# Kernel optimization log

Hardware: AMD Instinct MI355X
Metric: run time of the kernel (lower is better)

Reference implementation:

```python
import jax, jax.numpy as jnp
import numpy as np

B, D, H = 8192, 512, 512


def _linear_init(key, out_dim, in_dim, bias=True):
    # torch nn.Linear default: U(-1/sqrt(in_dim), 1/sqrt(in_dim)) for W and b
    k1, k2 = jax.random.split(key)
    bound = 1.0 / np.sqrt(in_dim)
    W = jax.random.uniform(k1, (out_dim, in_dim), jnp.float32, -bound, bound)
    if not bias:
        return W
    b = jax.random.uniform(k2, (out_dim,), jnp.float32, -bound, bound)
    return W, b


def setup_inputs() -> dict:
    key = jax.random.key(0)
    ks = jax.random.split(key, 16)
    x = jax.random.normal(ks[0], (B, D), jnp.float32)
    delta_t = jax.random.uniform(ks[1], (B, 1), jnp.float32)
    hidden = jax.random.normal(ks[2], (B, H), jnp.float32)
    cell_s = jax.random.normal(ks[3], (B, H), jnp.float32)
    Wii, bii = _linear_init(ks[4], H, D)
    Whi, bhi = _linear_init(ks[5], H, H)
    Wig, big = _linear_init(ks[6], H, D)
    Whg, bhg = _linear_init(ks[7], H, H)
    Wio, bio = _linear_init(ks[8], H, D)
    Who, bho = _linear_init(ks[9], H, H)
    Wto, bto = _linear_init(ks[10], H, 1)
    Wco, bco = _linear_init(ks[11], H, H)
    Wit1, bit1 = _linear_init(ks[12], H, D)
    Wtt1 = _linear_init(ks[13], H, 1, bias=False)
    Wit2, bit2 = _linear_init(ks[14], H, D)
    Wtt2 = _linear_init(ks[15], H, 1, bias=False)
    return dict(x=x, delta_t=delta_t, hidden=hidden, cell_s=cell_s,
                Wii=Wii, bii=bii, Whi=Whi, bhi=bhi, Wig=Wig, big=big,
                Whg=Whg, bhg=bhg, Wio=Wio, bio=bio, Who=Who, bho=bho,
                Wto=Wto, bto=bto, Wco=Wco, bco=bco, Wit1=Wit1, bit1=bit1,
                Wtt1=Wtt1, Wit2=Wit2, bit2=bit2, Wtt2=Wtt2)


def _lin(a, W, b=None):
    y = a @ W.T
    return y if b is None else y + b


def reference(x, delta_t, hidden, cell_s,
              Wii, bii, Whi, bhi, Wig, big, Whg, bhg,
              Wio, bio, Who, bho, Wto, bto, Wco, bco,
              Wit1, bit1, Wtt1, Wit2, bit2, Wtt2):
    sig, tanh = jax.nn.sigmoid, jnp.tanh
    tm1 = sig(_lin(x, Wit1, bit1) + sig(_lin(delta_t, Wtt1)))
    tm2 = sig(_lin(x, Wit2, bit2) + sig(_lin(delta_t, Wtt2)))
    im = sig(_lin(x, Wii, bii) + _lin(hidden, Whi, bhi))
    cur_in = tanh(_lin(x, Wig, big) + _lin(hidden, Whg, bhg))
    it1 = im * tm1
    cm_t = (1.0 - it1) * cell_s + it1 * cur_in
    cm = (1.0 - im) * cell_s + im * tm2 * cur_in
    om = sig(_lin(x, Wio, bio) + _lin(delta_t, Wto, bto)
             + _lin(hidden, Who, bho) + _lin(cm_t, Wco, bco))
    hm = om * tanh(cm_t)
    return (hm, cm)
```

## Files before the change

kernel.cpp:

```cpp
#include <hip/hip_runtime.h>
#include <hip/hip_bf16.h>
#include <stdint.h>

#define B_SZ 8192
#define D_SZ 512
#define H_SZ 512
#define KC 1024
#define NPRE 2560

typedef __attribute__((ext_vector_type(8))) __bf16 bf16x8;
typedef __attribute__((ext_vector_type(4))) float f32x4;

__device__ __forceinline__ unsigned short f2bf(float f) {
  unsigned u = __builtin_bit_cast(unsigned, f);
  u += 0x7FFFu + ((u >> 16) & 1u);
  return (unsigned short)(u >> 16);
}
__device__ __forceinline__ float bf2f(unsigned short h) {
  unsigned u = ((unsigned)h) << 16;
  return __builtin_bit_cast(float, u);
}
__device__ __forceinline__ float sigf(float x) {
  return __builtin_amdgcn_rcpf(1.0f + __expf(-x));
}
__device__ __forceinline__ float tanh_fast(float x) {
  float e = __expf(-2.0f * x);
  return (1.0f - e) * __builtin_amdgcn_rcpf(1.0f + e);
}

__device__ __forceinline__ void async_ld16(const unsigned short* g, unsigned short* l) {
  __builtin_amdgcn_global_load_lds(
      (const __attribute__((address_space(1))) unsigned int*)g,
      (__attribute__((address_space(3))) unsigned int*)l, 16, 0, 0);
}

struct WSrcs { const float* wx[5]; const float* wh[3]; const float* wco; };

__global__ void pack_all(const float* __restrict__ x, const float* __restrict__ h, WSrcs ws,
                         unsigned short* __restrict__ Ab, unsigned short* __restrict__ Wall,
                         unsigned short* __restrict__ Wcob) {
  int i = (blockIdx.x * 256 + threadIdx.x) * 4;
  const int XH = B_SZ * KC;
  const float* s;
  unsigned short* d;
  if (i < XH) {
    int b = i >> 10, c = i & 1023;
    s = (c < 512) ? (x + (size_t)b * 512 + c) : (h + (size_t)b * 512 + (c - 512));
    d = Ab + i;
  } else if (i < XH + NPRE * KC) {
    int j = i - XH;
    int row = j >> 10, c = j & 1023;
    int gate = row >> 9, r = row & 511;
    d = Wall + j;
    if (c < 512) {
      s = ws.wx[gate] + (size_t)r * 512 + c;
    } else if (gate >= 2) {
      s = ws.wh[gate - 2] + (size_t)r * 512 + (c - 512);
    } else {
      return;
    }
  } else {
    int j = i - XH - NPRE * KC;
    s = ws.wco + j;
    d = Wcob + j;
  }
  float4 v = *(const float4*)s;
  ushort4 o; o.x = f2bf(v.x); o.y = f2bf(v.y); o.z = f2bf(v.z); o.w = f2bf(v.w);
  *(ushort4*)d = o;
}

__global__ __launch_bounds__(640, 2) void igo_gate(
    const unsigned short* __restrict__ A, const unsigned short* __restrict__ Wall,
    const float* __restrict__ delta_t, const float* __restrict__ cell_s,
    const float* __restrict__ bii, const float* __restrict__ bhi,
    const float* __restrict__ big, const float* __restrict__ bhg,
    const float* __restrict__ bio, const float* __restrict__ bho,
    const float* __restrict__ Wto, const float* __restrict__ bto,
    const float* __restrict__ bco,
    const float* __restrict__ bit1, const float* __restrict__ Wtt1,
    const float* __restrict__ bit2, const float* __restrict__ Wtt2,
    float* __restrict__ out_cm, unsigned short* __restrict__ cmt_b,
    unsigned short* __restrict__ ao_b) {
  __shared__ __align__(16) unsigned short sBuf[28672];
  const int tid  = threadIdx.x;
  const int wave = tid >> 6, lane = tid & 63;
  const int ln15 = lane & 15, kq = lane >> 4;
  const int mh   = wave / 5, slot = wave % 5;
  const long bm  = (long)blockIdx.y * 128;
  const int  bn64 = blockIdx.x * 64;

  f32x4 acc[4][4];
#pragma unroll
  for (int i = 0; i < 4; ++i)
#pragma unroll
    for (int j = 0; j < 4; ++j) acc[i][j] = (f32x4){0.f, 0.f, 0.f, 0.f};

  const int swb = ln15 & 7;
  bf16x8* chunks = (bf16x8*)sBuf;

  for (int kt = 0; kt < 16; ++kt) {
    const int k0 = kt << 6;
    __syncthreads();
    const int cnt = (kt < 8) ? 3584 : 2560;
    for (int idx = tid; idx < cnt; idx += 640) {
      int t_lin = idx >> 9;
      int f     = idx & 511;
      int tile  = (kt < 8) ? t_lin : (t_lin < 2 ? t_lin : t_lin + 2);
      int row = f >> 3;
      int col = ((f & 7) ^ (row & 7)) << 3;
      const unsigned short* src;
      if (tile < 2) src = A    + (size_t)(bm + tile * 64 + row) * KC + k0 + col;
      else          src = Wall + (size_t)((tile - 2) * 512 + bn64 + row) * KC + k0 + col;
      async_ld16(src, sBuf + (size_t)(tile * 512 + f) * 8);
    }
    __syncthreads();
    if (kt < 8 || slot >= 2) {
#pragma unroll
      for (int ko = 0; ko < 2; ++ko) {
        const int q = (ko * 4 + kq) ^ swb;
        bf16x8 af[4], wf[4];
#pragma unroll
        for (int t = 0; t < 4; ++t)
          af[t] = chunks[mh * 512 + (t * 16 + ln15) * 8 + q];
#pragma unroll
        for (int t = 0; t < 4; ++t)
          wf[t] = chunks[(2 + slot) * 512 + (t * 16 + ln15) * 8 + q];
#pragma unroll
        for (int i = 0; i < 4; ++i)
#pragma unroll
          for (int j = 0; j < 4; ++j)
            acc[i][j] = __builtin_amdgcn_mfma_f32_16x16x32_bf16(af[i], wf[j], acc[i][j], 0, 0, 0);
      }
    }
  }

  for (int mh_e = 0; mh_e < 2; ++mh_e) {
    __syncthreads();
    if (mh == mh_e) {
#pragma unroll
      for (int i = 0; i < 4; ++i)
#pragma unroll
        for (int j = 0; j < 4; ++j)
#pragma unroll
          for (int r = 0; r < 4; ++r) {
            int row = i * 16 + kq * 4 + r;
            int col = j * 16 + ln15;
            sBuf[(size_t)slot * 4096 + row * 64 + col] = f2bf(acc[i][j][r]);
          }
    }
    __syncthreads();
    for (int v = tid; v < 1024; v += 640) {
      int row = v >> 4;
      int c4  = (v & 15) << 2;
      long b  = bm + mh_e * 64 + row;
      int  h  = bn64 + c4;
      int  lo = row * 64 + c4;
      ushort4 ut1 = *(const ushort4*)(sBuf + 0 * 4096 + lo);
      ushort4 ut2 = *(const ushort4*)(sBuf + 1 * 4096 + lo);
      ushort4 uai = *(const ushort4*)(sBuf + 2 * 4096 + lo);
      ushort4 uag = *(const ushort4*)(sBuf + 3 * 4096 + lo);
      ushort4 uao = *(const ushort4*)(sBuf + 4 * 4096 + lo);
      float4 cs   = *(const float4*)(cell_s + (size_t)b * 512 + h);
      float4 vbii = *(const float4*)(bii + h), vbhi = *(const float4*)(bhi + h);
      float4 vbig = *(const float4*)(big + h), vbhg = *(const float4*)(bhg + h);
      float4 vbio = *(const float4*)(bio + h), vbho = *(const float4*)(bho + h);
      float4 vWto = *(const float4*)(Wto + h), vbto = *(const float4*)(bto + h);
      float4 vbco = *(const float4*)(bco + h);
      float4 vbt1 = *(const float4*)(bit1 + h), vwt1 = *(const float4*)(Wtt1 + h);
      float4 vbt2 = *(const float4*)(bit2 + h), vwt2 = *(const float4*)(Wtt2 + h);
      float dtb   = delta_t[b];

      float4 ocm; ushort4 ocmt, oao;
#pragma unroll
      for (int l = 0; l < 4; ++l) {
        float t1 = sigf(bf2f(((const unsigned short*)&ut1)[l]) + ((const float*)&vbt1)[l]
                        + sigf(dtb * ((const float*)&vwt1)[l]));
        float t2 = sigf(bf2f(((const unsigned short*)&ut2)[l]) + ((const float*)&vbt2)[l]
                        + sigf(dtb * ((const float*)&vwt2)[l]));
        float ai = bf2f(((const unsigned short*)&uai)[l]) + ((const float*)&vbii)[l] + ((const float*)&vbhi)[l];
        float ag = bf2f(((const unsigned short*)&uag)[l]) + ((const float*)&vbig)[l] + ((const float*)&vbhg)[l];
        float ao = bf2f(((const unsigned short*)&uao)[l]) + ((const float*)&vbio)[l] + ((const float*)&vbho)[l]
                 + dtb * ((const float*)&vWto)[l] + ((const float*)&vbto)[l] + ((const float*)&vbco)[l];
        float im = sigf(ai);
        float g  = tanh_fast(ag);
        float csl = ((const float*)&cs)[l];
        float it1 = im * t1;
        float cmt = (1.f - it1) * csl + it1 * g;
        float cm  = (1.f - im) * csl + im * t2 * g;
        ((float*)&ocm)[l] = cm;
        ((unsigned short*)&ocmt)[l] = f2bf(cmt);
        ((unsigned short*)&oao)[l]  = f2bf(ao);
      }
      *(float4*)(out_cm + (size_t)b * 512 + h) = ocm;
      *(ushort4*)(cmt_b + (size_t)b * 512 + h) = ocmt;
      *(ushort4*)(ao_b  + (size_t)b * 512 + h) = oao;
    }
  }
}

__global__ __launch_bounds__(256, 2) void gemm_out(
    const unsigned short* __restrict__ A , const unsigned short* __restrict__ W ,
    const unsigned short* __restrict__ AO, float* __restrict__ out_hm) {
  __shared__ bf16x8 sA[128 * 8];
  __shared__ bf16x8 sW[128 * 8];
  const int tid  = threadIdx.x;
  const int wave = tid >> 6, lane = tid & 63;
  const int ln15 = lane & 15, kq = lane >> 4;
  const int wr = wave >> 1, wc = wave & 1;
  const long bm = (long)blockIdx.y * 128;
  const long bn = (long)blockIdx.x * 128;
  const int swb = ln15 & 7;

  f32x4 acc[4][4];
#pragma unroll
  for (int i = 0; i < 4; ++i)
#pragma unroll
    for (int j = 0; j < 4; ++j) acc[i][j] = (f32x4){0.f, 0.f, 0.f, 0.f};

  for (int kt = 0; kt < 8; ++kt) {
    const int k0 = kt << 6;
    __syncthreads();
#pragma unroll
    for (int it = 0; it < 4; ++it) {
      int f   = it * 256 + tid;
      int row = f >> 3;
      int col = ((f & 7) ^ (row & 7)) << 3;
      int ldsc = it * 256 + wave * 64;
      async_ld16(A + (size_t)(bm + row) * H_SZ + k0 + col, (unsigned short*)sA + (size_t)ldsc * 8);
      async_ld16(W + (size_t)(bn + row) * H_SZ + k0 + col, (unsigned short*)sW + (size_t)ldsc * 8);
    }
    __syncthreads();
#pragma unroll
    for (int ko = 0; ko < 2; ++ko) {
      const int q = (ko * 4 + kq) ^ swb;
      bf16x8 af[4], wf[4];
#pragma unroll
      for (int t = 0; t < 4; ++t)
        af[t] = sA[(wr * 64 + t * 16 + ln15) * 8 + q];
#pragma unroll
      for (int t = 0; t < 4; ++t)
        wf[t] = sW[(wc * 64 + t * 16 + ln15) * 8 + q];
#pragma unroll
      for (int i = 0; i < 4; ++i)
#pragma unroll
        for (int j = 0; j < 4; ++j)
          acc[i][j] = __builtin_amdgcn_mfma_f32_16x16x32_bf16(af[i], wf[j], acc[i][j], 0, 0, 0);
    }
  }
#pragma unroll
  for (int i = 0; i < 4; ++i) {
    const long r0 = bm + wr * 64 + i * 16 + kq * 4;
#pragma unroll
    for (int j = 0; j < 4; ++j) {
      const long c = bn + wc * 64 + j * 16 + ln15;
#pragma unroll
      for (int r = 0; r < 4; ++r) {
        long row = r0 + r;
        size_t idx = (size_t)row * H_SZ + c;
        float ao  = bf2f(AO[idx]);
        float om  = sigf(ao + acc[i][j][r]);
        float cmt = bf2f(A[idx]);
        out_hm[idx] = om * tanh_fast(cmt);
      }
    }
  }
}

extern "C" void kernel_launch(void* const* d_in, const int* in_sizes, int n_in,
                              void* d_out, int out_size, void* d_ws, size_t ws_size,
                              hipStream_t stream) {
  const float* x    = (const float*)d_in[0];
  const float* dt   = (const float*)d_in[1];
  const float* hid  = (const float*)d_in[2];
  const float* cell = (const float*)d_in[3];
  const float* Wii  = (const float*)d_in[4];
  const float* bii  = (const float*)d_in[5];
  const float* Whi  = (const float*)d_in[6];
  const float* bhi  = (const float*)d_in[7];
  const float* Wig  = (const float*)d_in[8];
  const float* big  = (const float*)d_in[9];
  const float* Whg  = (const float*)d_in[10];
  const float* bhg  = (const float*)d_in[11];
  const float* Wio  = (const float*)d_in[12];
  const float* bio  = (const float*)d_in[13];
  const float* Who  = (const float*)d_in[14];
  const float* bho  = (const float*)d_in[15];
  const float* Wto  = (const float*)d_in[16];
  const float* bto  = (const float*)d_in[17];
  const float* Wco  = (const float*)d_in[18];
  const float* bco  = (const float*)d_in[19];
  const float* Wit1 = (const float*)d_in[20];
  const float* bit1 = (const float*)d_in[21];
  const float* Wtt1 = (const float*)d_in[22];
  const float* Wit2 = (const float*)d_in[23];
  const float* bit2 = (const float*)d_in[24];
  const float* Wtt2 = (const float*)d_in[25];

  char* wp = (char*)d_ws;
  unsigned short* Ab   = (unsigned short*)wp; wp += (size_t)B_SZ * KC * 2;
  unsigned short* Wall = (unsigned short*)wp; wp += (size_t)NPRE * KC * 2;
  unsigned short* Wcob = (unsigned short*)wp; wp += (size_t)H_SZ * H_SZ * 2;
  unsigned short* Cmtb = (unsigned short*)wp; wp += (size_t)B_SZ * H_SZ * 2;
  unsigned short* AOb  = (unsigned short*)wp; wp += (size_t)B_SZ * H_SZ * 2;

  float* out = (float*)d_out;

  WSrcs wsrc;
  wsrc.wx[0] = Wit1; wsrc.wx[1] = Wit2; wsrc.wx[2] = Wii; wsrc.wx[3] = Wig; wsrc.wx[4] = Wio;
  wsrc.wh[0] = Whi;  wsrc.wh[1] = Whg;  wsrc.wh[2] = Who; wsrc.wco = Wco;
  const int pack_elems = B_SZ * KC + NPRE * KC + H_SZ * H_SZ;
  pack_all<<<pack_elems / 4 / 256, 256, 0, stream>>>(x, hid, wsrc, Ab, Wall, Wcob);

  igo_gate<<<dim3(8, 64), 640, 0, stream>>>(
      Ab, Wall, dt, cell, bii, bhi, big, bhg, bio, bho, Wto, bto, bco,
      bit1, Wtt1, bit2, Wtt2,
      out + (size_t)B_SZ * H_SZ, Cmtb, AOb);

  gemm_out<<<dim3(4, 64), 256, 0, stream>>>(Cmtb, Wcob, AOb, out);
}
```

Baseline: 251.6 us.

## Retile gate GEMM to 64-row blocks with 4 waves and XCD-aware block mapping

The gate kernel goes from 640-thread blocks covering 128 rows and 5 gate tiles to 256-thread blocks covering 64 rows. Three waves each compute one full-K gate (i, g, o), and a fourth wave computes the two half-K time gates with two accumulator sets, which aims to balance MFMA work across waves and raise occupancy. Both GEMM kernels now use a 1D grid whose block index is remapped by XCD, so neighbouring row tiles share an L2 and reuse weights. In exchange, the A tile is reloaded per 64 rows rather than shared across 128 rows, and wave 3 holds twice the accumulator registers.

```diff
diff --git a/kernel.cpp b/kernel.cpp
--- a/kernel.cpp
+++ b/kernel.cpp
@@ -69,7 +69,7 @@
   *(ushort4*)d = o;
 }
 
-__global__ __launch_bounds__(640, 2) void igo_gate(
+__global__ __launch_bounds__(256, 3) void fused_gate(
     const unsigned short* __restrict__ A, const unsigned short* __restrict__ Wall,
     const float* __restrict__ delta_t, const float* __restrict__ cell_s,
     const float* __restrict__ bii, const float* __restrict__ bhi,
@@ -81,19 +81,24 @@
     const float* __restrict__ bit2, const float* __restrict__ Wtt2,
     float* __restrict__ out_cm, unsigned short* __restrict__ cmt_b,
     unsigned short* __restrict__ ao_b) {
-  __shared__ __align__(16) unsigned short sBuf[28672];
+  __shared__ __align__(16) unsigned short sBuf[24576];
   const int tid  = threadIdx.x;
   const int wave = tid >> 6, lane = tid & 63;
   const int ln15 = lane & 15, kq = lane >> 4;
-  const int mh   = wave / 5, slot = wave % 5;
-  const long bm  = (long)blockIdx.y * 128;
-  const int  bn64 = blockIdx.x * 64;
-
-  f32x4 acc[4][4];
+  const int bid  = blockIdx.x;
+  const int xcd  = bid & 7, idx0 = bid >> 3;
+  const long bm  = (long)(xcd * 16 + (idx0 >> 3)) * 64;
+  const int  bn64 = (idx0 & 7) * 64;
+
+  f32x4 acc_a[4][4];
+  f32x4 acc_b[4][4];
 #pragma unroll
   for (int i = 0; i < 4; ++i)
 #pragma unroll
-    for (int j = 0; j < 4; ++j) acc[i][j] = (f32x4){0.f, 0.f, 0.f, 0.f};
+    for (int j = 0; j < 4; ++j) {
+      acc_a[i][j] = (f32x4){0.f, 0.f, 0.f, 0.f};
+      acc_b[i][j] = (f32x4){0.f, 0.f, 0.f, 0.f};
+    }
 
   const int swb = ln15 & 7;
   bf16x8* chunks = (bf16x8*)sBuf;
@@ -101,100 +106,139 @@
   for (int kt = 0; kt < 16; ++kt) {
     const int k0 = kt << 6;
     __syncthreads();
-    const int cnt = (kt < 8) ? 3584 : 2560;
-    for (int idx = tid; idx < cnt; idx += 640) {
-      int t_lin = idx >> 9;
-      int f     = idx & 511;
-      int tile  = (kt < 8) ? t_lin : (t_lin < 2 ? t_lin : t_lin + 2);
-      int row = f >> 3;
-      int col = ((f & 7) ^ (row & 7)) << 3;
-      const unsigned short* src;
-      if (tile < 2) src = A    + (size_t)(bm + tile * 64 + row) * KC + k0 + col;
-      else          src = Wall + (size_t)((tile - 2) * 512 + bn64 + row) * KC + k0 + col;
-      async_ld16(src, sBuf + (size_t)(tile * 512 + f) * 8);
+    if (kt < 8) {
+#pragma unroll
+      for (int it = 0; it < 12; ++it) {
+        int idx = it * 256 + tid;
+        int t = idx >> 9, f = idx & 511;
+        int row = f >> 3;
+        int col = ((f & 7) ^ (row & 7)) << 3;
+        const unsigned short* src;
+        if (t == 0) {
+          src = A + (size_t)(bm + row) * KC + k0 + col;
+        } else {
+          int rb = (t < 4) ? ((t + 1) << 9) : ((t - 4) << 9);
+          src = Wall + (size_t)(rb + bn64 + row) * KC + k0 + col;
+        }
+        async_ld16(src, sBuf + (size_t)idx * 8);
+      }
+    } else {
+#pragma unroll
+      for (int it = 0; it < 8; ++it) {
+        int idx = it * 256 + tid;
+        int t = idx >> 9, f = idx & 511;
+        int row = f >> 3;
+        int col = ((f & 7) ^ (row & 7)) << 3;
+        const unsigned short* src;
+        if (t == 0) src = A    + (size_t)(bm + row) * KC + k0 + col;
+        else        src = Wall + (size_t)(((t + 1) << 9) + bn64 + row) * KC + k0 + col;
+        async_ld16(src, sBuf + (size_t)idx * 8);
+      }
     }
     __syncthreads();
-    if (kt < 8 || slot >= 2) {
+    if (wave < 3) {
 #pragma unroll
       for (int ko = 0; ko < 2; ++ko) {
         const int q = (ko * 4 + kq) ^ swb;
         bf16x8 af[4], wf[4];
 #pragma unroll
         for (int t = 0; t < 4; ++t)
-          af[t] = chunks[mh * 512 + (t * 16 + ln15) * 8 + q];
+          af[t] = chunks[(t * 16 + ln15) * 8 + q];
 #pragma unroll
         for (int t = 0; t < 4; ++t)
-          wf[t] = chunks[(2 + slot) * 512 + (t * 16 + ln15) * 8 + q];
+          wf[t] = chunks[(1 + wave) * 512 + (t * 16 + ln15) * 8 + q];
 #pragma unroll
         for (int i = 0; i < 4; ++i)
 #pragma unroll
           for (int j = 0; j < 4; ++j)
-            acc[i][j] = __builtin_amdgcn_mfma_f32_16x16x32_bf16(af[i], wf[j], acc[i][j], 0, 0, 0);
-      }
-    }
-  }
-
-  for (int mh_e = 0; mh_e < 2; ++mh_e) {
-    __syncthreads();
-    if (mh == mh_e) {
-#pragma unroll
-      for (int i = 0; i < 4; ++i)
-#pragma unroll
-        for (int j = 0; j < 4; ++j)
-#pragma unroll
-          for (int r = 0; r < 4; ++r) {
-            int row = i * 16 + kq * 4 + r;
-            int col = j * 16 + ln15;
-            sBuf[(size_t)slot * 4096 + row * 64 + col] = f2bf(acc[i][j][r]);
+            acc_a[i][j] = __builtin_amdgcn_mfma_f32_16x16x32_bf16(af[i], wf[j], acc_a[i][j], 0, 0, 0);
+      }
+    } else if (kt < 8) {
+#pragma unroll
+      for (int ko = 0; ko < 2; ++ko) {
+        const int q = (ko * 4 + kq) ^ swb;
+        bf16x8 af[4], w1[4], w2[4];
+#pragma unroll
+        for (int t = 0; t < 4; ++t)
+          af[t] = chunks[(t * 16 + ln15) * 8 + q];
+#pragma unroll
+        for (int t = 0; t < 4; ++t) {
+          w1[t] = chunks[4 * 512 + (t * 16 + ln15) * 8 + q];
+          w2[t] = chunks[5 * 512 + (t * 16 + ln15) * 8 + q];
+        }
+#pragma unroll
+        for (int i = 0; i < 4; ++i)
+#pragma unroll
+          for (int j = 0; j < 4; ++j) {
+            acc_a[i][j] = __builtin_amdgcn_mfma_f32_16x16x32_bf16(af[i], w1[j], acc_a[i][j], 0, 0, 0);
+            acc_b[i][j] = __builtin_amdgcn_mfma_f32_16x16x32_bf16(af[i], w2[j], acc_b[i][j], 0, 0, 0);
           }
-    }
-    __syncthreads();
-    for (int v = tid; v < 1024; v += 640) {
-      int row = v >> 4;
-      int c4  = (v & 15) << 2;
-      long b  = bm + mh_e * 64 + row;
-      int  h  = bn64 + c4;
-      int  lo = row * 64 + c4;
-      ushort4 ut1 = *(const ushort4*)(sBuf + 0 * 4096 + lo);
-      ushort4 ut2 = *(const ushort4*)(sBuf + 1 * 4096 + lo);
-      ushort4 uai = *(const ushort4*)(sBuf + 2 * 4096 + lo);
-      ushort4 uag = *(const ushort4*)(sBuf + 3 * 4096 + lo);
-      ushort4 uao = *(const ushort4*)(sBuf + 4 * 4096 + lo);
-      float4 cs   = *(const float4*)(cell_s + (size_t)b * 512 + h);
-      float4 vbii = *(const float4*)(bii + h), vbhi = *(const float4*)(bhi + h);
-      float4 vbig = *(const float4*)(big + h), vbhg = *(const float4*)(bhg + h);
-      float4 vbio = *(const float4*)(bio + h), vbho = *(const float4*)(bho + h);
-      float4 vWto = *(const float4*)(Wto + h), vbto = *(const float4*)(bto + h);
-      float4 vbco = *(const float4*)(bco + h);
-      float4 vbt1 = *(const float4*)(bit1 + h), vwt1 = *(const float4*)(Wtt1 + h);
-      float4 vbt2 = *(const float4*)(bit2 + h), vwt2 = *(const float4*)(Wtt2 + h);
-      float dtb   = delta_t[b];
-
-      float4 ocm; ushort4 ocmt, oao;
-#pragma unroll
-      for (int l = 0; l < 4; ++l) {
-        float t1 = sigf(bf2f(((const unsigned short*)&ut1)[l]) + ((const float*)&vbt1)[l]
-                        + sigf(dtb * ((const float*)&vwt1)[l]));
-        float t2 = sigf(bf2f(((const unsigned short*)&ut2)[l]) + ((const float*)&vbt2)[l]
-                        + sigf(dtb * ((const float*)&vwt2)[l]));
-        float ai = bf2f(((const unsigned short*)&uai)[l]) + ((const float*)&vbii)[l] + ((const float*)&vbhi)[l];
-        float ag = bf2f(((const unsigned short*)&uag)[l]) + ((const float*)&vbig)[l] + ((const float*)&vbhg)[l];
-        float ao = bf2f(((const unsigned short*)&uao)[l]) + ((const float*)&vbio)[l] + ((const float*)&vbho)[l]
-                 + dtb * ((const float*)&vWto)[l] + ((const float*)&vbto)[l] + ((const float*)&vbco)[l];
-        float im = sigf(ai);
-        float g  = tanh_fast(ag);
-        float csl = ((const float*)&cs)[l];
-        float it1 = im * t1;
-        float cmt = (1.f - it1) * csl + it1 * g;
-        float cm  = (1.f - im) * csl + im * t2 * g;
-        ((float*)&ocm)[l] = cm;
-        ((unsigned short*)&ocmt)[l] = f2bf(cmt);
-        ((unsigned short*)&oao)[l]  = f2bf(ao);
-      }
-      *(float4*)(out_cm + (size_t)b * 512 + h) = ocm;
-      *(ushort4*)(cmt_b + (size_t)b * 512 + h) = ocmt;
-      *(ushort4*)(ao_b  + (size_t)b * 512 + h) = oao;
-    }
+      }
+    }
+  }
+
+  __syncthreads();
+#pragma unroll
+  for (int i = 0; i < 4; ++i)
+#pragma unroll
+    for (int j = 0; j < 4; ++j)
+#pragma unroll
+      for (int r = 0; r < 4; ++r) {
+        int row = i * 16 + kq * 4 + r;
+        int col = j * 16 + ln15;
+        sBuf[(size_t)wave * 4096 + row * 64 + col] = f2bf(acc_a[i][j][r]);
+        if (wave == 3)
+          sBuf[(size_t)4 * 4096 + row * 64 + col] = f2bf(acc_b[i][j][r]);
+      }
+  __syncthreads();
+
+#pragma unroll
+  for (int p = 0; p < 4; ++p) {
+    int v   = p * 256 + tid;
+    int row = v >> 4;
+    int c4  = (v & 15) << 2;
+    long b  = bm + row;
+    int  h  = bn64 + c4;
+    int  lo = row * 64 + c4;
+    ushort4 uai = *(const ushort4*)(sBuf + 0 * 4096 + lo);
+    ushort4 uag = *(const ushort4*)(sBuf + 1 * 4096 + lo);
+    ushort4 uao = *(const ushort4*)(sBuf + 2 * 4096 + lo);
+    ushort4 ut1 = *(const ushort4*)(sBuf + 3 * 4096 + lo);
+    ushort4 ut2 = *(const ushort4*)(sBuf + 4 * 4096 + lo);
+    float4 cs   = *(const float4*)(cell_s + (size_t)b * 512 + h);
+    float4 vbii = *(const float4*)(bii + h), vbhi = *(const float4*)(bhi + h);
+    float4 vbig = *(const float4*)(big + h), vbhg = *(const float4*)(bhg + h);
+    float4 vbio = *(const float4*)(bio + h), vbho = *(const float4*)(bho + h);
+    float4 vWto = *(const float4*)(Wto + h), vbto = *(const float4*)(bto + h);
+    float4 vbco = *(const float4*)(bco + h);
+    float4 vbt1 = *(const float4*)(bit1 + h), vwt1 = *(const float4*)(Wtt1 + h);
+    float4 vbt2 = *(const float4*)(bit2 + h), vwt2 = *(const float4*)(Wtt2 + h);
+    float dtb   = delta_t[b];
+
+    float4 ocm; ushort4 ocmt, oao;
+#pragma unroll
+    for (int l = 0; l < 4; ++l) {
+      float t1 = sigf(bf2f(((const unsigned short*)&ut1)[l]) + ((const float*)&vbt1)[l]
+                      + sigf(dtb * ((const float*)&vwt1)[l]));
+      float t2 = sigf(bf2f(((const unsigned short*)&ut2)[l]) + ((const float*)&vbt2)[l]
+                      + sigf(dtb * ((const float*)&vwt2)[l]));
+      float ai = bf2f(((const unsigned short*)&uai)[l]) + ((const float*)&vbii)[l] + ((const float*)&vbhi)[l];
+      float ag = bf2f(((const unsigned short*)&uag)[l]) + ((const float*)&vbig)[l] + ((const float*)&vbhg)[l];
+      float ao = bf2f(((const unsigned short*)&uao)[l]) + ((const float*)&vbio)[l] + ((const float*)&vbho)[l]
+               + dtb * ((const float*)&vWto)[l] + ((const float*)&vbto)[l] + ((const float*)&vbco)[l];
+      float im = sigf(ai);
+      float g  = tanh_fast(ag);
+      float csl = ((const float*)&cs)[l];
+      float it1 = im * t1;
+      float cmt = (1.f - it1) * csl + it1 * g;
+      float cm  = (1.f - im) * csl + im * t2 * g;
+      ((float*)&ocm)[l] = cm;
+      ((unsigned short*)&ocmt)[l] = f2bf(cmt);
+      ((unsigned short*)&oao)[l]  = f2bf(ao);
+    }
+    *(float4*)(out_cm + (size_t)b * 512 + h) = ocm;
+    *(ushort4*)(cmt_b + (size_t)b * 512 + h) = ocmt;
+    *(ushort4*)(ao_b  + (size_t)b * 512 + h) = oao;
   }
 }
 
@@ -207,8 +251,10 @@
   const int wave = tid >> 6, lane = tid & 63;
   const int ln15 = lane & 15, kq = lane >> 4;
   const int wr = wave >> 1, wc = wave & 1;
-  const long bm = (long)blockIdx.y * 128;
-  const long bn = (long)blockIdx.x * 128;
+  const int bid = blockIdx.x;
+  const int xcd = bid & 7, idx = bid >> 3;
+  const long bm = (long)(xcd * 8 + (idx >> 2)) * 128;
+  const long bn = (long)(idx & 3) * 128;
   const int swb = ln15 & 7;
 
   f32x4 acc[4][4];
@@ -256,11 +302,11 @@
 #pragma unroll
       for (int r = 0; r < 4; ++r) {
         long row = r0 + r;
-        size_t idx = (size_t)row * H_SZ + c;
-        float ao  = bf2f(AO[idx]);
+        size_t idx2 = (size_t)row * H_SZ + c;
+        float ao  = bf2f(AO[idx2]);
         float om  = sigf(ao + acc[i][j][r]);
-        float cmt = bf2f(A[idx]);
-        out_hm[idx] = om * tanh_fast(cmt);
+        float cmt = bf2f(A[idx2]);
+        out_hm[idx2] = om * tanh_fast(cmt);
       }
     }
   }
@@ -311,10 +357,10 @@
   const int pack_elems = B_SZ * KC + NPRE * KC + H_SZ * H_SZ;
   pack_all<<<pack_elems / 4 / 256, 256, 0, stream>>>(x, hid, wsrc, Ab, Wall, Wcob);
 
-  igo_gate<<<dim3(8, 64), 640, 0, stream>>>(
+  fused_gate<<<1024, 256, 0, stream>>>(
       Ab, Wall, dt, cell, bii, bhi, big, bhg, bio, bho, Wto, bto, bco,
       bit1, Wtt1, bit2, Wtt2,
       out + (size_t)B_SZ * H_SZ, Cmtb, AOb);
 
-  gemm_out<<<dim3(4, 64), 256, 0, stream>>>(Cmtb, Wcob, AOb, out);
-}
+  gemm_out<<<256, 256, 0, stream>>>(Cmtb, Wcob, AOb, out);
+}
```

Result: slower. 313.5 us (+24.6%).
